# Performance work log

Measured on AMD Instinct MI355X. Metric: run time of the kernel, lower is better.

Reference implementation:

```python
import jax, jax.numpy as jnp
import numpy as np

B, CB, FH, FW = 32, 512, 11, 20   # batch, backbone channels, fmap h/w (stride 32 on 360x640)
CAF, N, S = 64, 1000, 72          # anchor feat channels, n anchors, offsets
D = CAF * FH                      # 704, per-anchor flattened feature dim

# static off-diagonal indices for the attention matrix scatter
_ROWS, _COLS = np.nonzero(1 - np.eye(N))


def setup_inputs() -> dict:
    key = jax.random.key(0)
    ks = jax.random.split(key, 12)
    x = jax.random.normal(ks[0], (B, CB, FH, FW), jnp.float32)
    # structured anchor-cut indices, flat order iterates (anchor, channel, row)
    cut_zs = np.tile(np.repeat(np.arange(CAF), FH), N).astype(np.int32)
    cut_ys = np.tile(np.arange(FH), N * CAF).astype(np.int32)
    xs_nh = np.asarray(jax.random.randint(ks[1], (N, FH), -4, FW + 4))  # unclamped anchor x per (anchor,row)
    cut_xs = np.broadcast_to(np.clip(xs_nh, 0, FW - 1)[:, None, :], (N, CAF, FH)).reshape(-1).astype(np.int32)
    invalid_mask = jnp.asarray(((xs_nh < 0) | (xs_nh >= FW))[:, None, :])  # (N,1,FH), broadcast over channels
    sc = 0.02
    return {
        'x': x,
        'anchors': jax.random.normal(ks[2], (N, 5 + S), jnp.float32),
        'conv1_w': jax.random.normal(ks[3], (CAF, CB), jnp.float32) * sc,
        'conv1_b': jnp.zeros((CAF,), jnp.float32),
        'attn_w': jax.random.normal(ks[4], (N - 1, D), jnp.float32) * sc,
        'attn_b': jnp.zeros((N - 1,), jnp.float32),
        'cls_w': jax.random.normal(ks[5], (2, 2 * D), jnp.float32) * sc,
        'cls_b': jnp.zeros((2,), jnp.float32),
        'reg_w': jax.random.normal(ks[6], (S + 1, 2 * D), jnp.float32) * sc,
        'reg_b': jnp.zeros((S + 1,), jnp.float32),
        'cut_zs': jnp.asarray(cut_zs),
        'cut_ys': jnp.asarray(cut_ys),
        'cut_xs': jnp.asarray(cut_xs),
        'invalid_mask': invalid_mask,
    }


def reference(x, anchors, conv1_w, conv1_b, attn_w, attn_b, cls_w, cls_b,
              reg_w, reg_b, cut_zs, cut_ys, cut_xs, invalid_mask):
    # 1x1 conv == channel matmul
    feat = jnp.einsum('bchw,oc->bohw', x, conv1_w) + conv1_b[None, :, None, None]
    # irregular per-anchor gather: feat[b, cut_zs, cut_ys, cut_xs] -> (B, N*CAF*FH)
    rois = feat[:, cut_zs, cut_ys, cut_xs].reshape(B, N, CAF, FH)
    rois = jnp.where(invalid_mask[None], 0.0, rois)
    baf = rois.reshape(B, N, D)  # batch_anchor_features
    # attention over other anchors
    scores = jnp.einsum('bnd,md->bnm', baf, attn_w) + attn_b  # (B,N,N-1)
    attention = jax.nn.softmax(scores, axis=-1)
    # zero-diagonal attention matrix: off-diag entries filled row-major
    att_mat = jnp.zeros((B, N, N), feat.dtype).at[:, _ROWS, _COLS].set(attention.reshape(B, -1))
    att_feat = jnp.einsum('bnm,bmd->bnd', att_mat, baf)
    all_feat = jnp.concatenate([att_feat, baf], axis=-1)  # (B,N,2D)
    cls_logits = jnp.einsum('bnd,od->bno', all_feat, cls_w) + cls_b  # (B,N,2)
    reg = jnp.einsum('bnd,od->bno', all_feat, reg_w) + reg_b          # (B,N,S+1)
    # reg_proposals = anchors; [:, :2]=cls; [:, 4:]+=reg
    reg_proposals = jnp.concatenate(
        [cls_logits,
         jnp.broadcast_to(anchors[None, :, 2:4], (B, N, 2)),
         anchors[None, :, 4:] + reg], axis=-1)  # (B,N,77)
    return reg_proposals
```

## Files before the change

### kernel.cpp

```cpp
#include <hip/hip_runtime.h>


typedef unsigned short u16;
typedef short short8 __attribute__((ext_vector_type(8)));
typedef float f32x4 __attribute__((ext_vector_type(4)));

__device__ __forceinline__ u16 f2bf(float f) {
    union { float f; unsigned u; } v; v.f = f;
    unsigned r = v.u + 0x7FFFu + ((v.u >> 16) & 1u);
    return (u16)(r >> 16);
}
__device__ __forceinline__ float bf2f(u16 u) {
    union { unsigned u; float f; } v; v.u = ((unsigned)u) << 16;
    return v.f;
}

__device__ __forceinline__ void gload16(const u16* gsrc, u16* ldst) {
    __builtin_amdgcn_global_load_lds(
        (const __attribute__((address_space(1))) unsigned int*)gsrc,
        (__attribute__((address_space(3))) unsigned int*)ldst, 16, 0, 0);
}

#define DSR(d, a, off) asm volatile("ds_read_b128 %0, %1 offset:" #off : "=v"(d) : "v"(a))
#define LGKMN(n) do { asm volatile("s_waitcnt lgkmcnt(" #n ")" ::: "memory"); \
                      __builtin_amdgcn_sched_barrier(0); } while (0)
#define WVM(n) do { asm volatile("s_waitcnt vmcnt(" #n ")" ::: "memory"); \
                    __builtin_amdgcn_sched_barrier(0); } while (0)
#define BAR do { __builtin_amdgcn_s_barrier(); \
                 __builtin_amdgcn_sched_barrier(0); } while (0)

__global__ __launch_bounds__(512) void k_prep(const float* __restrict__ attn_w,
                                              const float* __restrict__ cls_w,
                                              const float* __restrict__ reg_w,
                                              const int* __restrict__ cut_xs,
                                              const void* __restrict__ mask,
                                              const float* __restrict__ attn_b,
                                              const float* __restrict__ x,
                                              const float* __restrict__ w1,
                                              const float* __restrict__ b1,
                                              u16* __restrict__ attn_wb,
                                              u16* __restrict__ wcat,
                                              int* __restrict__ xn,
                                              float* __restrict__ attn_bp,
                                              float* __restrict__ feat) {
    const int blk = blockIdx.x, tid = threadIdx.x;
    if (blk < 1408) {
        int i = blk * 512 + tid;
        int r = i / 704;
        attn_wb[i] = (r < 999) ? f2bf(attn_w[i]) : (u16)0;
        return;
    }
    if (blk < 1792) {
        int i = (blk - 1408) * 512 + tid;
        int o = i / 1536, k = i - o * 1536;
        int ksrc = -1;
        if (k < 704) ksrc = k;
        else if (k >= 768 && k < 1472) ksrc = k - 64;
        float v = 0.f;
        if (ksrc >= 0) {
            if (o < 2) v = cls_w[o * 1408 + ksrc];
            else if (o < 75) v = reg_w[(o - 2) * 1408 + ksrc];
        }
        wcat[i] = f2bf(v);
        return;
    }
    if (blk < 1814) {
        const unsigned char* m8 = (const unsigned char*)mask;
        int any = 0;
        for (int i = tid; i < 11000; i += 512)
            if ((i & 3) && m8[i]) any = 1;
        any = __any(any) ? 1 : 0;
        __shared__ int sh[8];
        if ((tid & 63) == 0) sh[tid >> 6] = any;
        __syncthreads();
        int isb8 = 0;
        #pragma unroll
        for (int q = 0; q < 8; ++q) isb8 |= sh[q];
        int i = (blk - 1792) * 512 + tid;
        if (i < 11000) {
            int inv = isb8 ? (int)m8[i] : ((const int*)mask)[i];
            int n = i / 11, y = i - n * 11;
            xn[i] = inv ? -1 : cut_xs[n * 704 + y];
        }
        return;
    }
    if (blk == 1814) {
        for (int c = tid; c < 1024; c += 512)
            attn_bp[c] = (c < 999) ? attn_b[c] : 0.f;
        return;
    }
    {
        __shared__ __attribute__((aligned(16))) float wlT[512][4];
        __shared__ float part[4][224];
        const int idx = blk - 1815;
        const int b = idx & 31, og = idx >> 5;
        for (int i = tid; i < 2048; i += 512) {
            int c = i >> 2, o = i & 3;
            wlT[c][o] = w1[(size_t)(og * 4 + o) * 512 + c];
        }
        __syncthreads();
        const int p = tid & 255, kh = tid >> 8;
        f32x4 acc = {0.f, 0.f, 0.f, 0.f};
        if (p < 220) {
            const float* xb = x + (size_t)b * 512 * 220 + kh * 256 * 220 + p;
            const f32x4* wv = (const f32x4*)&wlT[kh * 256][0];
            #pragma unroll 8
            for (int c = 0; c < 256; ++c) {
                float xv = xb[(size_t)c * 220];
                f32x4 wq = wv[c];
                acc[0] = fmaf(xv, wq[0], acc[0]);
                acc[1] = fmaf(xv, wq[1], acc[1]);
                acc[2] = fmaf(xv, wq[2], acc[2]);
                acc[3] = fmaf(xv, wq[3], acc[3]);
            }
        }
        if (kh == 1 && p < 220) {
            #pragma unroll
            for (int o = 0; o < 4; ++o) part[o][p] = acc[o];
        }
        __syncthreads();
        if (kh == 0 && p < 220) {
            float* fo = feat + (size_t)b * 14080 + (og * 4) * 220 + p;
            #pragma unroll
            for (int o = 0; o < 4; ++o)
                fo[(size_t)o * 220] = acc[o] + part[o][p] + b1[og * 4 + o];
        }
    }
}

__global__ __launch_bounds__(256) void k_gat(const float* __restrict__ feat,
                                             const int* __restrict__ xn,
                                             u16* __restrict__ af,
                                             u16* __restrict__ bafT) {
    __shared__ __attribute__((aligned(16))) u16 tl[64 * 64];
    const int mt = blockIdx.x & 15, dt = blockIdx.x >> 4;
    const int b = blockIdx.y;
    const int tid = threadIdx.x;
    const float* fb = feat + (size_t)b * 14080;
    #pragma unroll
    for (int h = 0; h < 2; ++h) {
        const int nl = (tid >> 3) + h * 32;
        const int n = mt * 64 + nl;
        const int dc = (tid & 7) * 8;
        const int d8 = dt * 64 + dc;
        short8 o = {0, 0, 0, 0, 0, 0, 0, 0};
        #pragma unroll
        for (int j = 0; j < 8; ++j) {
            int d = d8 + j;
            float v = 0.f;
            if (n < 1000 && d < 704) {
                int c = d / 11, y = d - c * 11;
                int xv = xn[n * 11 + y];
                if (xv >= 0) v = fb[c * 220 + y * 20 + xv];
            }
            o[j] = (short)f2bf(v);
        }
        *(short8*)&af[((size_t)(b * 1024 + n)) * 1536 + 768 + d8] = o;
        int key = ((nl >> 3) + nl) & 7;
        *(short8*)&tl[nl * 64 + (((tid & 7) ^ key) * 8)] = o;
    }
    __syncthreads();
    u16* dst = bafT + ((size_t)b * 768 + dt * 64) * 1024 + mt * 64;
    #pragma unroll
    for (int h = 0; h < 2; ++h) {
        int slot = h * 256 + tid;
        int dl = slot >> 3, m8 = (slot & 7) * 8;
        short8 v;
        #pragma unroll
        for (int j = 0; j < 8; ++j) {
            int m = m8 + j;
            int key = ((m >> 3) + m) & 7;
            v[j] = (short)tl[m * 64 + (((dl >> 3) ^ key) * 8) + (dl & 7)];
        }
        *(short8*)&dst[(size_t)dl * 1024 + m8] = v;
    }
}

__global__ __launch_bounds__(512, 4) void k_g8(const u16* __restrict__ A, long sAb, int lda,
                                               const u16* __restrict__ Bt, long sBb, int ldb,
                                               void* __restrict__ Cv, long sCb, int ldc,
                                               int ntN, int tpb, int nwg, int ks, int cf32,
                                               const float* __restrict__ bias) {
    __shared__ __attribute__((aligned(16))) u16 LDS[36864];
    const int bid = blockIdx.x;
    const int cpx = nwg >> 3;
    const int logical = (bid & 7) * cpx + (bid >> 3);
    const int batch = logical / tpb;
    const int t0 = logical - batch * tpb;
    const int tM = t0 / ntN, tN = t0 - tM * ntN;
    A  += (size_t)batch * sAb;
    Bt += (size_t)batch * sBb;

    const int tid = threadIdx.x;
    const int lane = tid & 63, w = tid >> 6;
    const int wr = w >> 1, wc = w & 1;
    const int l15 = lane & 15;
    const int lkswz = ((lane >> 4) ^ ((l15 >> 1) & 3)) * 8;
    const u16* Abase = A + (size_t)tM * 256 * lda;
    const u16* Bbase = Bt + (size_t)tN * 128 * ldb;
    const int srow = tid >> 2;
    const int sgc = (((tid & 3) ^ ((tid >> 3) & 3)) * 8);

    f32x4 acc[4][4] = {};

    auto SG = [&](int t) {
        const int s = (t % 3) * 12288;
        const u16* ga = Abase + (size_t)srow * lda + t * 32 + sgc;
        gload16(ga, &LDS[s + tid * 8]);
        gload16(ga + (size_t)128 * lda, &LDS[s + 4096 + tid * 8]);
        gload16(Bbase + (size_t)srow * ldb + t * 32 + sgc, &LDS[s + 8192 + tid * 8]);
    };

    SG(0);
    if (ks > 1) { SG(1); WVM(3); } else { WVM(0); }
    BAR;

    const unsigned aAl = (unsigned)(size_t)&LDS[(wr * 64 + l15) * 32 + lkswz];
    const unsigned aBl = (unsigned)(size_t)&LDS[8192 + (wc * 64 + l15) * 32 + lkswz];

    for (int t = 0; t < ks; ++t) {
        const unsigned sb = (unsigned)(t % 3) * 24576u;
        short8 av[4], bv[4];
        {
            unsigned aA = aAl + sb, aB = aBl + sb;
            DSR(bv[0], aB, 0); DSR(bv[1], aB, 1024); DSR(bv[2], aB, 2048); DSR(bv[3], aB, 3072);
            DSR(av[0], aA, 0); DSR(av[1], aA, 1024); DSR(av[2], aA, 2048); DSR(av[3], aA, 3072);
        }
        if (t + 2 < ks) SG(t + 2);
        LGKMN(2);
        __builtin_amdgcn_s_setprio(1);
        #pragma unroll
        for (int m = 0; m < 2; ++m)
            #pragma unroll
            for (int n = 0; n < 4; ++n)
                acc[m][n] = __builtin_amdgcn_mfma_f32_16x16x32_bf16(av[m], bv[n], acc[m][n], 0, 0, 0);
        __builtin_amdgcn_s_setprio(0);
        LGKMN(0);
        __builtin_amdgcn_s_setprio(1);
        #pragma unroll
        for (int m = 2; m < 4; ++m)
            #pragma unroll
            for (int n = 0; n < 4; ++n)
                acc[m][n] = __builtin_amdgcn_mfma_f32_16x16x32_bf16(av[m], bv[n], acc[m][n], 0, 0, 0);
        __builtin_amdgcn_s_setprio(0);
        if (t + 2 < ks) { WVM(3); } else if (t + 1 < ks) { WVM(0); }
        BAR;
    }

    const int rb = tM * 256 + wr * 64 + ((lane >> 4) << 2);
    const int cb = tN * 128 + wc * 64 + l15;
    if (cf32) {
        float* C = (float*)Cv + (size_t)batch * sCb;
        #pragma unroll
        for (int m = 0; m < 4; ++m)
            #pragma unroll
            for (int n = 0; n < 4; ++n)
                #pragma unroll
                for (int j = 0; j < 4; ++j)
                    C[(size_t)(rb + m * 16 + j) * ldc + cb + n * 16] = acc[m][n][j];
    } else {
        float bb[4] = {0.f, 0.f, 0.f, 0.f};
        if (bias) {
            #pragma unroll
            for (int n = 0; n < 4; ++n) bb[n] = bias[cb + n * 16];
        }
        u16* C = (u16*)Cv + (size_t)batch * sCb;
        #pragma unroll
        for (int m = 0; m < 4; ++m)
            #pragma unroll
            for (int n = 0; n < 4; ++n)
                #pragma unroll
                for (int j = 0; j < 4; ++j)
                    C[(size_t)(rb + m * 16 + j) * ldc + cb + n * 16] = f2bf(acc[m][n][j] + bb[n]);
    }
}

__global__ __launch_bounds__(512, 4) void k_g3(const u16* __restrict__ A, int lda,
                                               const u16* __restrict__ Bt,
                                               const float* __restrict__ anchors,
                                               const float* __restrict__ cls_b,
                                               const float* __restrict__ reg_b,
                                               float* __restrict__ out,
                                               int nwg, int ks) {
    __shared__ __attribute__((aligned(16))) u16 LDS[32768];
    const int bid = blockIdx.x;
    const int cpx = nwg >> 3;
    const int tM = (bid & 7) * cpx + (bid >> 3);
    const int tid = threadIdx.x;
    const int lane = tid & 63, w = tid >> 6;
    const int wr2 = w >> 2, wc2 = w & 3;
    const int l15 = lane & 15;
    const int lkswz = ((lane >> 4) ^ ((l15 >> 1) & 3)) * 8;
    const u16* Abase = A + (size_t)tM * 128 * lda;
    const int srow = tid >> 2;
    const int sgc = (((tid & 3) ^ ((tid >> 3) & 3)) * 8);

    f32x4 acc[4][2] = {};

    auto SGA = [&](int t, int kh) {
        const int base = ((t & 1) * 2 + kh) * 4096;
        gload16(Abase + (size_t)srow * lda + t * 64 + kh * 32 + sgc, &LDS[base + tid * 8]);
    };
    auto SGB = [&](int t, int kh) {
        const int base = 16384 + ((t & 1) * 2 + kh) * 4096;
        gload16(Bt + (size_t)srow * 1536 + t * 64 + kh * 32 + sgc, &LDS[base + tid * 8]);
    };

    SGA(0, 0); SGB(0, 0); SGA(0, 1); SGB(0, 1);
    if (ks > 1) { SGA(1, 0); SGB(1, 0); WVM(2); } else { WVM(0); }
    BAR;

    const unsigned aAl = (unsigned)(size_t)&LDS[(wr2 * 64 + l15) * 32 + lkswz];
    const unsigned aBl = (unsigned)(size_t)&LDS[16384 + (wc2 * 32 + l15) * 32 + lkswz];

    #define G3MF(i0, i1, A0, A1, B) do { \
        __builtin_amdgcn_s_setprio(1); \
        acc[i0][0] = __builtin_amdgcn_mfma_f32_16x16x32_bf16(A0, B[0], acc[i0][0], 0, 0, 0); \
        acc[i0][1] = __builtin_amdgcn_mfma_f32_16x16x32_bf16(A0, B[1], acc[i0][1], 0, 0, 0); \
        acc[i1][0] = __builtin_amdgcn_mfma_f32_16x16x32_bf16(A1, B[0], acc[i1][0], 0, 0, 0); \
        acc[i1][1] = __builtin_amdgcn_mfma_f32_16x16x32_bf16(A1, B[1], acc[i1][1], 0, 0, 0); \
        __builtin_amdgcn_s_setprio(0); } while (0)

    for (int t = 0; t < ks; ++t) {
        const unsigned bo = (unsigned)(t & 1) * 16384u;
        short8 a0, a1, a2, a3, bb[2];
        if (t + 1 < ks) { SGA(t + 1, 1); SGB(t + 1, 1); }
        {
            unsigned aA = aAl + bo, aB = aBl + bo;
            DSR(bb[0], aB, 0); DSR(bb[1], aB, 1024);
            DSR(a0, aA, 0); DSR(a1, aA, 1024);
            DSR(a2, aA, 2048); DSR(a3, aA, 3072);
        }
        LGKMN(2);
        G3MF(0, 1, a0, a1, bb);
        LGKMN(0);
        BAR;
        if (t + 2 < ks) SGA(t + 2, 0);
        G3MF(2, 3, a2, a3, bb);
        {
            unsigned aA = aAl + bo + 8192u, aB = aBl + bo + 8192u;
            DSR(bb[0], aB, 0); DSR(bb[1], aB, 1024);
            DSR(a0, aA, 0); DSR(a1, aA, 1024);
            DSR(a2, aA, 2048); DSR(a3, aA, 3072);
        }
        LGKMN(2);
        G3MF(0, 1, a0, a1, bb);
        LGKMN(0);
        BAR;
        if (t + 2 < ks) SGB(t + 2, 0);
        G3MF(2, 3, a2, a3, bb);
        if (t + 2 < ks) { WVM(2); } else if (t + 1 < ks) { WVM(0); }
        BAR;
    }
    #undef G3MF

    const int rb = tM * 128 + wr2 * 64 + ((lane >> 4) << 2);
    const int o = wc2 * 32 + l15;
    #pragma unroll
    for (int m = 0; m < 4; ++m) {
        #pragma unroll
        for (int n = 0; n < 2; ++n) {
            int oc = o + n * 16;
            #pragma unroll
            for (int j = 0; j < 4; ++j) {
                int r = rb + m * 16 + j;
                int b = r >> 10, nn = r & 1023;
                if (nn < 1000) {
                    float v = acc[m][n][j];
                    float* orow = out + ((size_t)b * 1000 + nn) * 77;
                    if (oc < 2) {
                        orow[oc] = v + cls_b[oc];
                    } else if (oc < 75) {
                        orow[oc + 2] = v + reg_b[oc - 2] + anchors[nn * 77 + oc + 2];
                        if (oc == 2) orow[2] = anchors[nn * 77 + 2];
                        if (oc == 3) orow[3] = anchors[nn * 77 + 3];
                    }
                }
            }
        }
    }
}

__global__ __launch_bounds__(256) void k_softmax(u16* __restrict__ att) {
    const int tid = threadIdx.x;
    const int lane = tid & 63;
    const int w = blockIdx.x * 4 + (tid >> 6);
    const int co0 = lane * 8, co1 = 512 + lane * 8;

    short8 c0, c1;
    {
        int b = w / 1000, n = w - b * 1000;
        const u16* rp = att + ((size_t)(b * 1024 + n)) * 1024;
        c0 = *(const short8*)&rp[co0];
        c1 = *(const short8*)&rp[co1];
    }
    for (int k = 0; k < 4; ++k) {
        const int idx = w + k * 8000;
        const int b = idx / 1000, n = idx - b * 1000;
        u16* rp = att + ((size_t)(b * 1024 + n)) * 1024;
        short8 d0 = c0, d1 = c1;
        if (k < 3) {
            int i2 = w + (k + 1) * 8000;
            int b2 = i2 / 1000, n2 = i2 - b2 * 1000;
            const u16* rp2 = att + ((size_t)(b2 * 1024 + n2)) * 1024;
            c0 = *(const short8*)&rp2[co0];
            c1 = *(const short8*)&rp2[co1];
        }
        float f0[8], f1[8];
        float m = -1e30f;
        #pragma unroll
        for (int j = 0; j < 8; ++j) {
            f0[j] = bf2f((u16)d0[j]);
            m = fmaxf(m, f0[j]);
        }
        #pragma unroll
        for (int j = 0; j < 8; ++j) {
            f1[j] = (co1 + j < 999) ? bf2f((u16)d1[j]) : -1e30f;
            m = fmaxf(m, f1[j]);
        }
        #pragma unroll
        for (int o = 32; o > 0; o >>= 1) m = fmaxf(m, __shfl_xor(m, o));
        float e0[8], e1[8];
        float s = 0.f;
        #pragma unroll
        for (int j = 0; j < 8; ++j) { e0[j] = __expf(f0[j] - m); s += e0[j]; }
        #pragma unroll
        for (int j = 0; j < 8; ++j) {
            e1[j] = (co1 + j < 999) ? __expf(f1[j] - m) : 0.f;
            s += e1[j];
        }
        #pragma unroll
        for (int o = 32; o > 0; o >>= 1) s += __shfl_xor(s, o);
        const float inv = 1.f / s;
        float p0 = __shfl_up(e0[7], 1);
        float p1 = __shfl_up(e1[7], 1);
        float x63 = __shfl(e0[7], 63);
        if (lane == 0) p1 = x63;
        short8 o0, o1;
        #pragma unroll
        for (int j = 0; j < 8; ++j) {
            int c = co0 + j;
            float pm = (j == 0) ? p0 : e0[j - 1];
            float val = (c < n) ? e0[j] : ((c > n) ? pm : 0.f);
            o0[j] = (short)f2bf(val * inv);
        }
        #pragma unroll
        for (int j = 0; j < 8; ++j) {
            int c = co1 + j;
            float pm = (j == 0) ? p1 : e1[j - 1];
            float val = 0.f;
            if (c < 1000) val = (c < n) ? e1[j] : ((c > n) ? pm : 0.f);
            o1[j] = (short)f2bf(val * inv);
        }
        *(short8*)&rp[co0] = o0;
        *(short8*)&rp[co1] = o1;
    }
}

extern "C" void kernel_launch(void* const* d_in, const int* in_sizes, int n_in,
                              void* d_out, int out_size, void* d_ws, size_t ws_size,
                              hipStream_t stream) {
    const float* x       = (const float*)d_in[0];
    const float* anchors = (const float*)d_in[1];
    const float* conv1_w = (const float*)d_in[2];
    const float* conv1_b = (const float*)d_in[3];
    const float* attn_w  = (const float*)d_in[4];
    const float* attn_b  = (const float*)d_in[5];
    const float* cls_w   = (const float*)d_in[6];
    const float* cls_b   = (const float*)d_in[7];
    const float* reg_w   = (const float*)d_in[8];
    const float* reg_b   = (const float*)d_in[9];
    const int*   cut_xs  = (const int*)d_in[12];
    const void*  invalid = d_in[13];
    float* out = (float*)d_out;

    char* ws = (char*)d_ws;
    u16*   wcat    = (u16*)  (ws + 0);
    u16*   attn_wb = (u16*)  (ws + 393216);
    u16*   af      = (u16*)  (ws + 1835008);
    u16*   bafT    = (u16*)  (ws + 102498304);
    u16*   att     = (u16*)  (ws + 152829952);
    float* feat    = (float*)(ws + 152829952);
    int*   xn      = (int*)  (ws + 154632192);
    float* attn_bp = (float*)(ws + 219938816);

    k_prep<<<2327, 512, 0, stream>>>(attn_w, cls_w, reg_w, cut_xs, invalid, attn_b,
                                     x, conv1_w, conv1_b,
                                     attn_wb, wcat, xn, attn_bp, feat);
    k_gat<<<dim3(192, 32), 256, 0, stream>>>(feat, xn, af, bafT);
    k_g8<<<1024, 512, 0, stream>>>(af + 768, 0L, 1536, attn_wb, 0L, 704,
                                   att, 0L, 1024, 8, 1024, 1024, 22, 0, attn_bp);
    k_softmax<<<2000, 256, 0, stream>>>(att);
    k_g8<<<768, 512, 0, stream>>>(att, 1048576L, 1024, bafT, 786432L, 1024,
                                  af, 1572864L, 1536, 6, 24, 768, 32, 0, nullptr);
    k_g3<<<256, 512, 0, stream>>>(af, 1536, wcat, anchors, cls_b, reg_b, out, 256, 24);
}
```

Measured before the change: 218.5 us.

## Widen final head GEMM to 1024 threads and skip padded K tiles

The final classification/regression GEMM now runs with 1024 threads per workgroup. Half the threads stage A tiles and half stage B tiles, and each wave computes a 32x32 output instead of 64x32, which doubles the wave count for latency hiding. The K loop is fixed at 22 tiles and skips physical tile 11, which appears to be padding between the two 704-wide halves of the concatenated features, cutting MFMA work and loads. The loop is also simplified to one load per half-step with a single barrier per half. The fixed trip count and skipped tile hard-code the layout, and the larger workgroup may limit occupancy.

```diff
diff --git a/kernel.cpp b/kernel.cpp
--- a/kernel.cpp
+++ b/kernel.cpp
@@ -275,13 +275,13 @@
     }
 }
 
-__global__ __launch_bounds__(512, 4) void k_g3(const u16* __restrict__ A, int lda,
-                                               const u16* __restrict__ Bt,
-                                               const float* __restrict__ anchors,
-                                               const float* __restrict__ cls_b,
-                                               const float* __restrict__ reg_b,
-                                               float* __restrict__ out,
-                                               int nwg, int ks) {
+__global__ __launch_bounds__(1024, 4) void k_g3(const u16* __restrict__ A, int lda,
+                                                const u16* __restrict__ Bt,
+                                                const float* __restrict__ anchors,
+                                                const float* __restrict__ cls_b,
+                                                const float* __restrict__ reg_b,
+                                                float* __restrict__ out,
+                                                int nwg) {
     __shared__ __attribute__((aligned(16))) u16 LDS[32768];
     const int bid = blockIdx.x;
     const int cpx = nwg >> 3;
@@ -292,72 +292,68 @@
     const int l15 = lane & 15;
     const int lkswz = ((lane >> 4) ^ ((l15 >> 1) & 3)) * 8;
     const u16* Abase = A + (size_t)tM * 128 * lda;
-    const int srow = tid >> 2;
-    const int sgc = (((tid & 3) ^ ((tid >> 3) & 3)) * 8);
-
-    f32x4 acc[4][2] = {};
-
-    auto SGA = [&](int t, int kh) {
-        const int base = ((t & 1) * 2 + kh) * 4096;
-        gload16(Abase + (size_t)srow * lda + t * 64 + kh * 32 + sgc, &LDS[base + tid * 8]);
+    const int stid = tid & 511;
+    const int srow = stid >> 2;
+    const int sgc = (((stid & 3) ^ ((stid >> 3) & 3)) * 8);
+    const bool isA = tid < 512;
+
+    f32x4 acc[2][2] = {};
+
+    auto SG = [&](int lt, int kh) {
+        const int pt = lt + (lt >= 11);
+        const int base = ((lt & 1) * 2 + kh) * 4096;
+        if (isA)
+            gload16(Abase + (size_t)srow * lda + pt * 64 + kh * 32 + sgc,
+                    &LDS[base + stid * 8]);
+        else
+            gload16(Bt + (size_t)srow * 1536 + pt * 64 + kh * 32 + sgc,
+                    &LDS[16384 + base + stid * 8]);
     };
-    auto SGB = [&](int t, int kh) {
-        const int base = 16384 + ((t & 1) * 2 + kh) * 4096;
-        gload16(Bt + (size_t)srow * 1536 + t * 64 + kh * 32 + sgc, &LDS[base + tid * 8]);
-    };
-
-    SGA(0, 0); SGB(0, 0); SGA(0, 1); SGB(0, 1);
-    if (ks > 1) { SGA(1, 0); SGB(1, 0); WVM(2); } else { WVM(0); }
+
+    SG(0, 0); SG(0, 1); SG(1, 0);
+    WVM(1);
     BAR;
 
-    const unsigned aAl = (unsigned)(size_t)&LDS[(wr2 * 64 + l15) * 32 + lkswz];
+    const unsigned aAl = (unsigned)(size_t)&LDS[(wr2 * 32 + l15) * 32 + lkswz];
     const unsigned aBl = (unsigned)(size_t)&LDS[16384 + (wc2 * 32 + l15) * 32 + lkswz];
 
-    #define G3MF(i0, i1, A0, A1, B) do { \
+    #define G3MM(B0, B1, A0, A1) do { \
         __builtin_amdgcn_s_setprio(1); \
-        acc[i0][0] = __builtin_amdgcn_mfma_f32_16x16x32_bf16(A0, B[0], acc[i0][0], 0, 0, 0); \
-        acc[i0][1] = __builtin_amdgcn_mfma_f32_16x16x32_bf16(A0, B[1], acc[i0][1], 0, 0, 0); \
-        acc[i1][0] = __builtin_amdgcn_mfma_f32_16x16x32_bf16(A1, B[0], acc[i1][0], 0, 0, 0); \
-        acc[i1][1] = __builtin_amdgcn_mfma_f32_16x16x32_bf16(A1, B[1], acc[i1][1], 0, 0, 0); \
+        acc[0][0] = __builtin_amdgcn_mfma_f32_16x16x32_bf16(A0, B0, acc[0][0], 0, 0, 0); \
+        acc[0][1] = __builtin_amdgcn_mfma_f32_16x16x32_bf16(A0, B1, acc[0][1], 0, 0, 0); \
+        acc[1][0] = __builtin_amdgcn_mfma_f32_16x16x32_bf16(A1, B0, acc[1][0], 0, 0, 0); \
+        acc[1][1] = __builtin_amdgcn_mfma_f32_16x16x32_bf16(A1, B1, acc[1][1], 0, 0, 0); \
         __builtin_amdgcn_s_setprio(0); } while (0)
 
-    for (int t = 0; t < ks; ++t) {
+    for (int t = 0; t < 22; ++t) {
         const unsigned bo = (unsigned)(t & 1) * 16384u;
-        short8 a0, a1, a2, a3, bb[2];
-        if (t + 1 < ks) { SGA(t + 1, 1); SGB(t + 1, 1); }
+        short8 a0, a1, b0, b1;
+        if (t + 1 < 22) SG(t + 1, 1);
         {
             unsigned aA = aAl + bo, aB = aBl + bo;
-            DSR(bb[0], aB, 0); DSR(bb[1], aB, 1024);
+            DSR(b0, aB, 0); DSR(b1, aB, 1024);
             DSR(a0, aA, 0); DSR(a1, aA, 1024);
-            DSR(a2, aA, 2048); DSR(a3, aA, 3072);
-        }
-        LGKMN(2);
-        G3MF(0, 1, a0, a1, bb);
+        }
         LGKMN(0);
+        G3MM(b0, b1, a0, a1);
         BAR;
-        if (t + 2 < ks) SGA(t + 2, 0);
-        G3MF(2, 3, a2, a3, bb);
+        if (t + 2 < 22) SG(t + 2, 0);
         {
             unsigned aA = aAl + bo + 8192u, aB = aBl + bo + 8192u;
-            DSR(bb[0], aB, 0); DSR(bb[1], aB, 1024);
+            DSR(b0, aB, 0); DSR(b1, aB, 1024);
             DSR(a0, aA, 0); DSR(a1, aA, 1024);
-            DSR(a2, aA, 2048); DSR(a3, aA, 3072);
-        }
-        LGKMN(2);
-        G3MF(0, 1, a0, a1, bb);
+        }
         LGKMN(0);
+        G3MM(b0, b1, a0, a1);
+        if (t + 2 < 22) { WVM(1); } else if (t + 1 < 22) { WVM(0); }
         BAR;
-        if (t + 2 < ks) SGB(t + 2, 0);
-        G3MF(2, 3, a2, a3, bb);
-        if (t + 2 < ks) { WVM(2); } else if (t + 1 < ks) { WVM(0); }
-        BAR;
-    }
-    #undef G3MF
-
-    const int rb = tM * 128 + wr2 * 64 + ((lane >> 4) << 2);
+    }
+    #undef G3MM
+
+    const int rb = tM * 128 + wr2 * 32 + ((lane >> 4) << 2);
     const int o = wc2 * 32 + l15;
     #pragma unroll
-    for (int m = 0; m < 4; ++m) {
+    for (int m = 0; m < 2; ++m) {
         #pragma unroll
         for (int n = 0; n < 2; ++n) {
             int oc = o + n * 16;
@@ -493,5 +489,5 @@
     k_softmax<<<2000, 256, 0, stream>>>(att);
     k_g8<<<768, 512, 0, stream>>>(att, 1048576L, 1024, bafT, 786432L, 1024,
                                   af, 1572864L, 1536, 6, 24, 768, 32, 0, nullptr);
-    k_g3<<<256, 512, 0, stream>>>(af, 1536, wcat, anchors, cls_b, reg_b, out, 256, 24);
-}
+    k_g3<<<256, 1024, 0, stream>>>(af, 1536, wcat, anchors, cls_b, reg_b, out, 256);
+}
```

Measured after the change: 215.3 us (median of 2 runs). About the same (-1.5%).
